# Kernel tuning notes

Hardware: AMD Instinct MI355X
Metric: run time of the kernel (lower is better)

## Reference

```python
import jax, jax.numpy as jnp
import numpy as np

D = 256      # d_model
SUB = 3      # number of adjacency subsets
GROUPS = 8
N, T, V = 32, 256, 19


def setup_inputs() -> dict:
    key = jax.random.key(0)
    ks = jax.random.split(key, 4)
    return {
        "x": jax.random.normal(ks[0], (N, T, V, D), jnp.float32),
        "para": jax.random.normal(ks[1], (3, GROUPS, V, V), jnp.float32),
        "linear_weight": jax.random.normal(ks[2], (D, D * SUB), jnp.float32) * 0.05,
        "linear_bias": jax.random.normal(ks[3], (1, D * SUB, 1, 1), jnp.float32) * 0.05,
        "bn_gamma": jnp.ones((D * SUB,), jnp.float32),
        "bn_beta": jnp.zeros((D * SUB,), jnp.float32),
        "bn1_gamma": jnp.ones((D,), jnp.float32),
        "bn1_beta": jnp.zeros((D,), jnp.float32),
    }


def _bn(x, gamma, beta, eps=1e-5):
    # BatchNorm2d (training mode): stats over (n, t, v) per channel
    m = jnp.mean(x, axis=(0, 2, 3), keepdims=True)
    v = jnp.var(x, axis=(0, 2, 3), keepdims=True)
    return (x - m) * jax.lax.rsqrt(v + eps) * gamma[None, :, None, None] + beta[None, :, None, None]


def reference(x, para, linear_weight, linear_bias, bn_gamma, bn_beta, bn1_gamma, bn1_beta):
    xc = jnp.transpose(x, (0, 3, 1, 2))                 # (n, c, t, v)
    # expand per-group adjacency to per-channel: (3, D, V, V)
    A = jnp.tile(para, (1, D // GROUPS, 1, 1))
    # L2 row-normalize along last dim (matches torch.norm(dim=-1))
    A = A / (jnp.linalg.norm(A, axis=-1, keepdims=True) + 1e-4)
    # channel mixing: (n, 3c, t, v)
    y = jnp.einsum('nctw,cd->ndtw', xc, linear_weight)
    y = _bn(y + linear_bias, bn_gamma, bn_beta)
    n, kc, t, v = y.shape
    y = y.reshape(n, SUB, kc // SUB, t, v)              # (n, k, c, t, v)
    # per-channel tiny 19x19 adjacency matmul
    y = jnp.einsum('nkctv,kcvw->nctw', y, A)            # (n, c, t, v)
    out = jax.nn.relu(_bn(y + xc, bn1_gamma, bn1_beta))
    return jnp.transpose(out, (0, 2, 3, 1))             # (n, t, v, c)
```

## Files before the change

kernel.cpp:

```cpp
#include <hip/hip_runtime.h>

typedef unsigned short u16;
typedef unsigned int u32;
typedef float f32x4 __attribute__((ext_vector_type(4)));
typedef __bf16 bf16x8 __attribute__((ext_vector_type(8)));

#define M_ALL 155648.0f
#define XP 264
#define YBP 152
#define ATP 72
#define ZBP 153

__device__ __forceinline__ u16 f2bf(float f) {
  union { float f; u32 u; } x; x.f = f;
  u32 u = x.u;
  u += 0x7FFFu + ((u >> 16) & 1u);
  return (u16)(u >> 16);
}
__device__ __forceinline__ float bf2f(u16 h) {
  union { u32 u; float f; } x; x.u = ((u32)h) << 16;
  return x.f;
}
__device__ __forceinline__ f32x4 zero4() { f32x4 z = {0.f, 0.f, 0.f, 0.f}; return z; }

__global__ void k_prep(const float* __restrict__ para, u16* __restrict__ wa,
                       float* __restrict__ stats) {
  int tid = threadIdx.x;
  for (int i = tid; i < 2048; i += 512) stats[i] = 0.f;
  if (tid < 456) {
    int k = tid / 152, rem = tid % 152, g = rem / 19, v = rem % 19;
    int base = ((k * 8 + g) * 19 + v) * 19;
    float ss = 0.f;
    #pragma unroll
    for (int w = 0; w < 19; ++w) { float a = para[base + w]; ss += a * a; }
    float inv = 1.f / (sqrtf(ss) + 1e-4f);
    #pragma unroll
    for (int w = 0; w < 19; ++w) wa[base + w] = f2bf(para[base + w] * inv);
  }
}

__global__ void k_wt(const float* __restrict__ W, u16* __restrict__ wt) {
  int idx = blockIdx.x * 512 + threadIdx.x;
  int d = idx >> 8, c = idx & 255;
  wt[idx] = f2bf(W[c * 768 + d]);
}

__global__ __launch_bounds__(512, 2) void k_stats(const float* __restrict__ x,
                                                  const u16* __restrict__ wt,
                                                  float* __restrict__ sumy) {
  __shared__ u16 xs[152 * XP];
  __shared__ float scr[768];
  int tid = threadIdx.x;
  int bid = blockIdx.x;
  int n = bid >> 5, tg = bid & 31;
  const float* xbase = x + (size_t)(n * 256 + tg * 8) * 4864;

  {
    int r = tid >> 6, c4 = (tid & 63) << 2;
    for (int it = 0; it < 19; ++it) {
      int m = it * 8 + r;
      float4 f = *reinterpret_cast<const float4*>(xbase + m * 256 + c4);
      uint2 p;
      p.x = (u32)f2bf(f.x) | ((u32)f2bf(f.y) << 16);
      p.y = (u32)f2bf(f.z) | ((u32)f2bf(f.w) << 16);
      *reinterpret_cast<uint2*>(&xs[m * XP + c4]) = p;
    }
  }
  __syncthreads();

  int lane = tid & 63, wave = tid >> 6;
  int mhalf = wave & 1, nt3 = wave >> 1;
  int cl = lane & 15, q = lane >> 4;
  const bf16x8* wtv = reinterpret_cast<const bf16x8*>(wt);
  int arow[5];
  #pragma unroll
  for (int i = 0; i < 5; ++i) {
    int rr = mhalf * 80 + i * 16 + cl;
    arow[i] = (rr > 151 ? 151 : rr) * XP;
  }
  float msk4 = (mhalf == 1 && q >= 2) ? 0.f : 1.f;

  for (int nc = 0; nc < 4; ++nc) {
    f32x4 acc[5][3];
    #pragma unroll
    for (int i = 0; i < 5; ++i)
      #pragma unroll
      for (int jj = 0; jj < 3; ++jj) acc[i][jj] = zero4();

    for (int s = 0; s < 8; ++s) {
      int kof = s * 32 + q * 8;
      bf16x8 b[3];
      #pragma unroll
      for (int jj = 0; jj < 3; ++jj) {
        int j = nt3 * 3 + jj;
        int d = (j >> 2) * 256 + nc * 64 + (j & 3) * 16 + cl;
        b[jj] = wtv[d * 32 + s * 4 + q];
      }
      #pragma unroll
      for (int i = 0; i < 5; ++i) {
        bf16x8 a = *reinterpret_cast<const bf16x8*>(&xs[arow[i] + kof]);
        #pragma unroll
        for (int jj = 0; jj < 3; ++jj)
          acc[i][jj] = __builtin_amdgcn_mfma_f32_16x16x32_bf16(a, b[jj], acc[i][jj], 0, 0, 0);
      }
    }
    #pragma unroll
    for (int jj = 0; jj < 3; ++jj) {
      float ps = 0.f, qs = 0.f;
      #pragma unroll
      for (int i = 0; i < 5; ++i) {
        float im = (i == 4) ? msk4 : 1.f;
        #pragma unroll
        for (int r = 0; r < 4; ++r) { float v = acc[i][jj][r] * im; ps += v; qs += v * v; }
      }
      ps += __shfl_xor(ps, 16); ps += __shfl_xor(ps, 32);
      qs += __shfl_xor(qs, 16); qs += __shfl_xor(qs, 32);
      if (lane < 16) { scr[wave * 96 + jj * 32 + lane] = ps; scr[wave * 96 + jj * 32 + 16 + lane] = qs; }
    }
    __syncthreads();
    if (tid < 384) {
      int nt = tid / 96, r = tid % 96, jj = r / 32, comp = (r & 31) >> 4, l = r & 15;
      int a0 = (2 * nt) * 96 + jj * 32 + comp * 16 + l;
      float val = scr[a0] + scr[a0 + 96];
      int j = nt * 3 + jj;
      int d = (j >> 2) * 256 + nc * 64 + (j & 3) * 16 + l;
      atomicAdd(&sumy[comp * 768 + d], val);
    }
    __syncthreads();
  }
}

__global__ void k_f1(const float* __restrict__ stats, const float* __restrict__ gam,
                     const float* __restrict__ bet, float* __restrict__ ST) {
  int d = threadIdx.x;
  float inv = 1.f / M_ALL;
  float mr = stats[d] * inv;
  float qv = stats[768 + d] * inv;
  float var = qv - mr * mr;
  float Sc = gam[d] * rsqrtf(var + 1e-5f);
  ST[d] = Sc;
  ST[768 + d] = bet[d] - mr * Sc;
}

__global__ __launch_bounds__(512, 2) void k_main(const float* __restrict__ x,
                                                 const u16* __restrict__ wt,
                                                 const u16* __restrict__ wa,
                                                 const float* __restrict__ ST,
                                                 float* __restrict__ sumz,
                                                 float* __restrict__ out) {
  __shared__ u16 xs[152 * XP];
  __shared__ u16 yb[3 * 64 * YBP];
  __shared__ u16 at[8 * 20 * ATP];
  int tid = threadIdx.x;
  int bid = blockIdx.x;
  int n = bid >> 5, tg = bid & 31;
  const float* xbase = x + (size_t)(n * 256 + tg * 8) * 4864;
  size_t obase = (size_t)(n * 256 + tg * 8) * 4864;

  for (int i = tid; i < 8 * 20 * ATP; i += 512) {
    int g = i / (20 * ATP), r = i % (20 * ATP), w = r / ATP, kv = r % ATP;
    u16 val = 0;
    if (w < 19 && kv < 57) {
      int k = kv / 19, v = kv - 19 * k;
      val = wa[((k * 8 + g) * 19 + v) * 19 + w];
    }
    at[i] = val;
  }
  {
    int r = tid >> 6, c4 = (tid & 63) << 2;
    for (int it = 0; it < 19; ++it) {
      int m = it * 8 + r;
      float4 f = *reinterpret_cast<const float4*>(xbase + m * 256 + c4);
      uint2 p;
      p.x = (u32)f2bf(f.x) | ((u32)f2bf(f.y) << 16);
      p.y = (u32)f2bf(f.z) | ((u32)f2bf(f.w) << 16);
      *reinterpret_cast<uint2*>(&xs[m * XP + c4]) = p;
    }
  }
  __syncthreads();

  int lane = tid & 63, wave = tid >> 6;
  int mhalf = wave & 1, nt3 = wave >> 1;
  int cl = lane & 15, q = lane >> 4;
  int g = wave;
  const bf16x8* wtv = reinterpret_cast<const bf16x8*>(wt);
  float* scrz = reinterpret_cast<float*>(&yb[9792]);
  u16* zbuf = yb;
  int arow[5];
  #pragma unroll
  for (int i = 0; i < 5; ++i) {
    int rr = mhalf * 80 + i * 16 + cl;
    arow[i] = (rr > 151 ? 151 : rr) * XP;
  }
  int aoff[2][8];
  #pragma unroll
  for (int ks = 0; ks < 2; ++ks)
    #pragma unroll
    for (int e = 0; e < 8; ++e) {
      int kv = ks * 32 + q * 8 + e;
      if (kv > 56) kv = 0;
      int k = kv / 19, v = kv - 19 * k;
      aoff[ks][e] = k * (64 * YBP) + v;
    }

  for (int nc = 0; nc < 4; ++nc) {
    f32x4 acc[5][3];
    #pragma unroll
    for (int i = 0; i < 5; ++i)
      #pragma unroll
      for (int jj = 0; jj < 3; ++jj) acc[i][jj] = zero4();
    for (int s = 0; s < 8; ++s) {
      int kof = s * 32 + q * 8;
      bf16x8 b[3];
      #pragma unroll
      for (int jj = 0; jj < 3; ++jj) {
        int j = nt3 * 3 + jj;
        int d = (j >> 2) * 256 + nc * 64 + (j & 3) * 16 + cl;
        b[jj] = wtv[d * 32 + s * 4 + q];
      }
      #pragma unroll
      for (int i = 0; i < 5; ++i) {
        bf16x8 a = *reinterpret_cast<const bf16x8*>(&xs[arow[i] + kof]);
        #pragma unroll
        for (int jj = 0; jj < 3; ++jj)
          acc[i][jj] = __builtin_amdgcn_mfma_f32_16x16x32_bf16(a, b[jj], acc[i][jj], 0, 0, 0);
      }
    }
    __syncthreads();

    #pragma unroll
    for (int jj = 0; jj < 3; ++jj) {
      int j = nt3 * 3 + jj;
      int ksub = j >> 2;
      int d = ksub * 256 + nc * 64 + (j & 3) * 16 + cl;
      float Sc = ST[d], Tc = ST[768 + d];
      int clloc = (j & 3) * 16 + cl;
      #pragma unroll
      for (int i = 0; i < 5; ++i) {
        int m = mhalf * 80 + i * 16 + q * 4;
        if (m < 152) {
          uint2 p;
          float v0 = acc[i][jj][0] * Sc + Tc;
          float v1 = acc[i][jj][1] * Sc + Tc;
          float v2 = acc[i][jj][2] * Sc + Tc;
          float v3 = acc[i][jj][3] * Sc + Tc;
          p.x = (u32)f2bf(v0) | ((u32)f2bf(v1) << 16);
          p.y = (u32)f2bf(v2) | ((u32)f2bf(v3) << 16);
          *reinterpret_cast<uint2*>(&yb[(ksub * 64 + clloc) * YBP + m]) = p;
        }
      }
    }
    __syncthreads();

    f32x4 zacc[4][2];
    #pragma unroll
    for (int mt = 0; mt < 4; ++mt) { zacc[mt][0] = zero4(); zacc[mt][1] = zero4(); }
    #pragma unroll
    for (int ks = 0; ks < 2; ++ks) {
      bf16x8 bfr[2];
      #pragma unroll
      for (int nt = 0; nt < 2; ++nt) {
        int w = nt * 16 + cl; if (w > 19) w = 19;
        bfr[nt] = *reinterpret_cast<const bf16x8*>(&at[(g * 20 + w) * ATP + ks * 32 + q * 8]);
      }
      #pragma unroll
      for (int mt = 0; mt < 4; ++mt) {
        int tc = mt * 16 + cl;
        int t = tc >> 3, c8 = tc & 7;
        int ybase = (c8 * 8 + g) * YBP + t * 19;
        union { bf16x8 v; u16 u[8]; } afr;
        #pragma unroll
        for (int e = 0; e < 8; ++e) afr.u[e] = yb[aoff[ks][e] + ybase];
        #pragma unroll
        for (int nt = 0; nt < 2; ++nt)
          zacc[mt][nt] = __builtin_amdgcn_mfma_f32_16x16x32_bf16(afr.v, bfr[nt], zacc[mt][nt], 0, 0, 0);
      }
    }
    __syncthreads();

    #pragma unroll
    for (int mt = 0; mt < 4; ++mt)
      #pragma unroll
      for (int nt = 0; nt < 2; ++nt)
        #pragma unroll
        for (int r = 0; r < 4; ++r) {
          int w = nt * 16 + cl;
          if (w < 19) {
            int tc = mt * 16 + q * 4 + r;
            int t = tc >> 3, c8 = tc & 7;
            zbuf[(c8 * 8 + g) * ZBP + t * 19 + w] = f2bf(zacc[mt][nt][r]);
          }
        }
    __syncthreads();

    float sz = 0.f, sq = 0.f;
    int cloc = tid & 63;
    int cglob = nc * 64 + cloc;
    #pragma unroll 1
    for (int rep = 0; rep < 19; ++rep) {
      int idx = rep * 512 + tid;
      int mp = idx >> 6;
      float z = bf2f(zbuf[cloc * ZBP + mp]) + bf2f(xs[mp * XP + cglob]);
      out[obase + (size_t)mp * 256 + cglob] = z;
      sz += z; sq += z * z;
    }
    scrz[cloc * 8 + (tid >> 6)] = sz;
    scrz[512 + cloc * 8 + (tid >> 6)] = sq;
    __syncthreads();
    if (tid < 128) {
      int comp = tid >> 6, c = tid & 63;
      float v = 0.f;
      #pragma unroll
      for (int h = 0; h < 8; ++h) v += scrz[comp * 512 + c * 8 + h];
      atomicAdd(&sumz[comp * 256 + nc * 64 + c], v);
    }
  }
}

__global__ void k_f2(const float* __restrict__ statz, const float* __restrict__ gam,
                     const float* __restrict__ bet, float* __restrict__ S1T1) {
  int c = threadIdx.x;
  float inv = 1.f / M_ALL;
  float mz = statz[c] * inv;
  float qv = statz[256 + c] * inv;
  float var = qv - mz * mz;
  float Sc = gam[c] * rsqrtf(var + 1e-5f);
  S1T1[c] = Sc;
  S1T1[256 + c] = bet[c] - mz * Sc;
}

__global__ __launch_bounds__(256) void k_relu(float* __restrict__ out,
                                              const float* __restrict__ S1T1) {
  int tid = threadIdx.x;
  int lane = tid & 63;
  int wv = ((blockIdx.x << 8) + tid) >> 6;
  const float4* s14 = reinterpret_cast<const float4*>(S1T1);
  float4 sv = s14[lane], tv = s14[64 + lane];
  float4* o4 = reinterpret_cast<float4*>(out);
  #pragma unroll 1
  for (int r = 0; r < 19; ++r) {
    size_t i = ((size_t)r * 8192 + wv) * 64 + lane;
    float4 f = o4[i];
    f.x = fmaxf(f.x * sv.x + tv.x, 0.f);
    f.y = fmaxf(f.y * sv.y + tv.y, 0.f);
    f.z = fmaxf(f.z * sv.z + tv.z, 0.f);
    f.w = fmaxf(f.w * sv.w + tv.w, 0.f);
    o4[i] = f;
  }
}

extern "C" void kernel_launch(void* const* d_in, const int* in_sizes, int n_in,
                              void* d_out, int out_size, void* d_ws, size_t ws_size,
                              hipStream_t stream) {
  const float* x    = (const float*)d_in[0];
  const float* para = (const float*)d_in[1];
  const float* W    = (const float*)d_in[2];
  const float* bng  = (const float*)d_in[4];
  const float* bnb  = (const float*)d_in[5];
  const float* bn1g = (const float*)d_in[6];
  const float* bn1b = (const float*)d_in[7];
  float* out = (float*)d_out;

  char* ws = (char*)d_ws;
  u16* wt    = (u16*)ws;
  u16* wa    = (u16*)(ws + 393216);
  float* st  = (float*)(ws + 410560);
  float* sumy = st;
  float* sumz = st + 1536;
  float* ST   = (float*)(ws + 418752);
  float* S1T1 = (float*)(ws + 424896);

  k_prep<<<dim3(1),    dim3(512), 0, stream>>>(para, wa, st);
  k_wt  <<<dim3(384),  dim3(512), 0, stream>>>(W, wt);
  k_stats<<<dim3(1024), dim3(512), 0, stream>>>(x, wt, sumy);
  k_f1  <<<dim3(1),    dim3(768), 0, stream>>>(sumy, bng, bnb, ST);
  k_main<<<dim3(1024), dim3(512), 0, stream>>>(x, wt, wa, ST, sumz, out);
  k_f2  <<<dim3(1),    dim3(256), 0, stream>>>(sumz, bn1g, bn1b, S1T1);
  k_relu<<<dim3(2048), dim3(256), 0, stream>>>(out, S1T1);
}
```

Baseline: 697.9 us.

## Compute first BN stats via Gram matrix of x and swizzle shared layouts

Replaces the statistics pass, which ran the full x·W GEMM just to get per-channel mean and variance, with a 256x256 Gram matrix of x plus column sums. Mean and variance of y are then derived as W^T colsum and w^T G w in small follow-up kernels (k_sym, k_f1). The main kernel also moves to XOR-swizzled LDS layouts for xs and for a new y2 buffer, so the adjacency-matmul A operand becomes one vector load instead of eight scalar gathers. The adjacency B fragments are preloaded into registers once. The risk is a different rounding path for the variance (bf16 Gram accumulated in fp32 with atomics) and the extra small kernels and memset.

```diff
diff --git a/kernel.cpp b/kernel.cpp
--- a/kernel.cpp
+++ b/kernel.cpp
@@ -6,10 +6,7 @@
 typedef __bf16 bf16x8 __attribute__((ext_vector_type(8)));
 
 #define M_ALL 155648.0f
-#define XP 264
-#define YBP 152
-#define ATP 72
-#define ZBP 153
+#define GP 168
 
 __device__ __forceinline__ u16 f2bf(float f) {
   union { float f; u32 u; } x; x.f = f;
@@ -23,10 +20,17 @@
 }
 __device__ __forceinline__ f32x4 zero4() { f32x4 z = {0.f, 0.f, 0.f, 0.f}; return z; }
 
-__global__ void k_prep(const float* __restrict__ para, u16* __restrict__ wa,
-                       float* __restrict__ stats) {
+__device__ __forceinline__ int xs_idx(int m, int c) {
+  return m * 256 + ((((c >> 3) ^ (m & 7)) << 3) | (c & 7));
+}
+__device__ __forceinline__ int y2_idx(int r, int kvp) {
+  int sw = (r & 7) ^ ((r >> 3) & 7);
+  return r * 64 + ((((kvp >> 3) ^ sw) << 3) | (kvp & 7));
+}
+
+__global__ void k_prep(const float* __restrict__ para, u16* __restrict__ wa2) {
+  __shared__ float aL[3 * 8 * 19 * 19];
   int tid = threadIdx.x;
-  for (int i = tid; i < 2048; i += 512) stats[i] = 0.f;
   if (tid < 456) {
     int k = tid / 152, rem = tid % 152, g = rem / 19, v = rem % 19;
     int base = ((k * 8 + g) * 19 + v) * 19;
@@ -35,7 +39,17 @@
     for (int w = 0; w < 19; ++w) { float a = para[base + w]; ss += a * a; }
     float inv = 1.f / (sqrtf(ss) + 1e-4f);
     #pragma unroll
-    for (int w = 0; w < 19; ++w) wa[base + w] = f2bf(para[base + w] * inv);
+    for (int w = 0; w < 19; ++w) aL[base + w] = para[base + w] * inv;
+  }
+  __syncthreads();
+  for (int i = tid; i < 8 * 20 * 64; i += 512) {
+    int g = i / 1280, rem = i % 1280, w = rem >> 6, kvp = rem & 63;
+    u16 val = 0;
+    if (w < 19 && kvp < 57) {
+      int k = kvp / 19, v = kvp - 19 * k;
+      val = f2bf(aL[((k * 8 + g) * 19 + v) * 19 + w]);
+    }
+    wa2[i] = val;
   }
 }
 
@@ -45,15 +59,129 @@
   wt[idx] = f2bf(W[c * 768 + d]);
 }
 
-__global__ __launch_bounds__(512, 2) void k_stats(const float* __restrict__ x,
-                                                  const u16* __restrict__ wt,
-                                                  float* __restrict__ sumy) {
-  __shared__ u16 xs[152 * XP];
-  __shared__ float scr[768];
+__global__ __launch_bounds__(512, 2) void k_gram(const float* __restrict__ x,
+                                                 float* __restrict__ G,
+                                                 float* __restrict__ colsum) {
+  __shared__ u16 xsT[256 * GP];
+  __shared__ float scs[512];
+  int tid = threadIdx.x, bid = blockIdx.x;
+  int c = tid & 255, mh = tid >> 8;
+  int lane = tid & 63, wave = tid >> 6;
+  int cl = lane & 15, q = lane >> 4;
+
+  if (tid < 256) {
+    *reinterpret_cast<uint2*>(&xsT[tid * GP + 152]) = make_uint2(0u, 0u);
+    *reinterpret_cast<uint2*>(&xsT[tid * GP + 156]) = make_uint2(0u, 0u);
+  }
+
+  float cs = 0.f;
+  f32x4 acc[2][16];
+  #pragma unroll
+  for (int ri = 0; ri < 2; ++ri)
+    #pragma unroll
+    for (int j = 0; j < 16; ++j) acc[ri][j] = zero4();
+
+  for (int ss = 0; ss < 4; ++ss) {
+    int sl = bid * 4 + ss;
+    const float* xb = x + (size_t)sl * 152 * 256;
+    __syncthreads();
+    #pragma unroll 1
+    for (int it = 0; it < 19; ++it) {
+      int m0 = it * 8 + mh * 4;
+      float v0 = xb[(m0 + 0) * 256 + c];
+      float v1 = xb[(m0 + 1) * 256 + c];
+      float v2 = xb[(m0 + 2) * 256 + c];
+      float v3 = xb[(m0 + 3) * 256 + c];
+      cs += v0 + v1 + v2 + v3;
+      uint2 p;
+      p.x = (u32)f2bf(v0) | ((u32)f2bf(v1) << 16);
+      p.y = (u32)f2bf(v2) | ((u32)f2bf(v3) << 16);
+      *reinterpret_cast<uint2*>(&xsT[c * GP + m0]) = p;
+    }
+    __syncthreads();
+    #pragma unroll
+    for (int s = 0; s < 5; ++s) {
+      int kof = s * 32 + q * 8;
+      bf16x8 a0 = *reinterpret_cast<const bf16x8*>(&xsT[(wave * 16 + cl) * GP + kof]);
+      bf16x8 a1 = *reinterpret_cast<const bf16x8*>(&xsT[((wave + 8) * 16 + cl) * GP + kof]);
+      #pragma unroll
+      for (int ct2 = 0; ct2 < 16; ++ct2) {
+        bf16x8 b = *reinterpret_cast<const bf16x8*>(&xsT[(ct2 * 16 + cl) * GP + kof]);
+        acc[0][ct2] = __builtin_amdgcn_mfma_f32_16x16x32_bf16(a0, b, acc[0][ct2], 0, 0, 0);
+        acc[1][ct2] = __builtin_amdgcn_mfma_f32_16x16x32_bf16(a1, b, acc[1][ct2], 0, 0, 0);
+      }
+    }
+  }
+  #pragma unroll
+  for (int ri = 0; ri < 2; ++ri) {
+    int ct = wave + ri * 8;
+    #pragma unroll
+    for (int ct2 = 0; ct2 < 16; ++ct2) {
+      if (ct2 >= ct) {
+        #pragma unroll
+        for (int r4 = 0; r4 < 4; ++r4)
+          atomicAdd(&G[(ct * 16 + q * 4 + r4) * 256 + ct2 * 16 + cl], acc[ri][ct2][r4]);
+      }
+    }
+  }
+  scs[tid] = cs;
+  __syncthreads();
+  if (tid < 256) atomicAdd(&colsum[tid], scs[tid] + scs[tid + 256]);
+}
+
+__global__ void k_sym(float* __restrict__ G) {
+  int i = blockIdx.x * 256 + threadIdx.x;
+  int r = i >> 8, cN = i & 255;
+  if (r > cN) G[i] = G[cN * 256 + r];
+}
+
+__global__ __launch_bounds__(256) void k_f1(const float* __restrict__ G,
+                                            const float* __restrict__ colsum,
+                                            const float* __restrict__ W,
+                                            const float* __restrict__ gam,
+                                            const float* __restrict__ bet,
+                                            float* __restrict__ ST) {
+  __shared__ float wd[256];
+  __shared__ float red[16];
+  int d = blockIdx.x, c = threadIdx.x;
+  float wv = W[c * 768 + d];
+  wd[c] = wv;
+  __syncthreads();
+  float dot = 0.f;
+  const float* Gr = G + c * 256;
+  #pragma unroll 4
+  for (int j = 0; j < 256; ++j) dot += Gr[j] * wd[j];
+  float part = wv * dot;
+  float mpart = colsum[c] * wv;
+  #pragma unroll
+  for (int o = 32; o; o >>= 1) { part += __shfl_down(part, o); mpart += __shfl_down(mpart, o); }
+  int lane = c & 63, w = c >> 6;
+  if (lane == 0) { red[w] = part; red[8 + w] = mpart; }
+  __syncthreads();
+  if (c == 0) {
+    float qv = red[0] + red[1] + red[2] + red[3];
+    float ms = red[8] + red[9] + red[10] + red[11];
+    float mean = ms / M_ALL;
+    float var = qv / M_ALL - mean * mean;
+    float S = gam[d] * rsqrtf(var + 1e-5f);
+    ST[d] = S;
+    ST[768 + d] = bet[d] - mean * S;
+  }
+}
+
+__global__ __launch_bounds__(512, 2) void k_main(const float* __restrict__ x,
+                                                 const u16* __restrict__ wt,
+                                                 const u16* __restrict__ wa2,
+                                                 const float* __restrict__ ST,
+                                                 float* __restrict__ sumz,
+                                                 float* __restrict__ out) {
+  __shared__ u16 xs[152 * 256];
+  __shared__ u16 y2[512 * 64];
+  __shared__ float scrz[1024];
   int tid = threadIdx.x;
   int bid = blockIdx.x;
-  int n = bid >> 5, tg = bid & 31;
-  const float* xbase = x + (size_t)(n * 256 + tg * 8) * 4864;
+  const float* xbase = x + (size_t)bid * 152 * 256;
+  size_t obase = (size_t)bid * 152 * 256;
 
   {
     int r = tid >> 6, c4 = (tid & 63) << 2;
@@ -63,145 +191,34 @@
       uint2 p;
       p.x = (u32)f2bf(f.x) | ((u32)f2bf(f.y) << 16);
       p.y = (u32)f2bf(f.z) | ((u32)f2bf(f.w) << 16);
-      *reinterpret_cast<uint2*>(&xs[m * XP + c4]) = p;
-    }
-  }
-  __syncthreads();
-
-  int lane = tid & 63, wave = tid >> 6;
-  int mhalf = wave & 1, nt3 = wave >> 1;
-  int cl = lane & 15, q = lane >> 4;
-  const bf16x8* wtv = reinterpret_cast<const bf16x8*>(wt);
-  int arow[5];
-  #pragma unroll
-  for (int i = 0; i < 5; ++i) {
-    int rr = mhalf * 80 + i * 16 + cl;
-    arow[i] = (rr > 151 ? 151 : rr) * XP;
-  }
-  float msk4 = (mhalf == 1 && q >= 2) ? 0.f : 1.f;
-
-  for (int nc = 0; nc < 4; ++nc) {
-    f32x4 acc[5][3];
-    #pragma unroll
-    for (int i = 0; i < 5; ++i)
-      #pragma unroll
-      for (int jj = 0; jj < 3; ++jj) acc[i][jj] = zero4();
-
-    for (int s = 0; s < 8; ++s) {
-      int kof = s * 32 + q * 8;
-      bf16x8 b[3];
-      #pragma unroll
-      for (int jj = 0; jj < 3; ++jj) {
-        int j = nt3 * 3 + jj;
-        int d = (j >> 2) * 256 + nc * 64 + (j & 3) * 16 + cl;
-        b[jj] = wtv[d * 32 + s * 4 + q];
-      }
-      #pragma unroll
-      for (int i = 0; i < 5; ++i) {
-        bf16x8 a = *reinterpret_cast<const bf16x8*>(&xs[arow[i] + kof]);
-        #pragma unroll
-        for (int jj = 0; jj < 3; ++jj)
-          acc[i][jj] = __builtin_amdgcn_mfma_f32_16x16x32_bf16(a, b[jj], acc[i][jj], 0, 0, 0);
-      }
-    }
-    #pragma unroll
-    for (int jj = 0; jj < 3; ++jj) {
-      float ps = 0.f, qs = 0.f;
-      #pragma unroll
-      for (int i = 0; i < 5; ++i) {
-        float im = (i == 4) ? msk4 : 1.f;
-        #pragma unroll
-        for (int r = 0; r < 4; ++r) { float v = acc[i][jj][r] * im; ps += v; qs += v * v; }
-      }
-      ps += __shfl_xor(ps, 16); ps += __shfl_xor(ps, 32);
-      qs += __shfl_xor(qs, 16); qs += __shfl_xor(qs, 32);
-      if (lane < 16) { scr[wave * 96 + jj * 32 + lane] = ps; scr[wave * 96 + jj * 32 + 16 + lane] = qs; }
-    }
-    __syncthreads();
-    if (tid < 384) {
-      int nt = tid / 96, r = tid % 96, jj = r / 32, comp = (r & 31) >> 4, l = r & 15;
-      int a0 = (2 * nt) * 96 + jj * 32 + comp * 16 + l;
-      float val = scr[a0] + scr[a0 + 96];
-      int j = nt * 3 + jj;
-      int d = (j >> 2) * 256 + nc * 64 + (j & 3) * 16 + l;
-      atomicAdd(&sumy[comp * 768 + d], val);
-    }
-    __syncthreads();
-  }
-}
-
-__global__ void k_f1(const float* __restrict__ stats, const float* __restrict__ gam,
-                     const float* __restrict__ bet, float* __restrict__ ST) {
-  int d = threadIdx.x;
-  float inv = 1.f / M_ALL;
-  float mr = stats[d] * inv;
-  float qv = stats[768 + d] * inv;
-  float var = qv - mr * mr;
-  float Sc = gam[d] * rsqrtf(var + 1e-5f);
-  ST[d] = Sc;
-  ST[768 + d] = bet[d] - mr * Sc;
-}
-
-__global__ __launch_bounds__(512, 2) void k_main(const float* __restrict__ x,
-                                                 const u16* __restrict__ wt,
-                                                 const u16* __restrict__ wa,
-                                                 const float* __restrict__ ST,
-                                                 float* __restrict__ sumz,
-                                                 float* __restrict__ out) {
-  __shared__ u16 xs[152 * XP];
-  __shared__ u16 yb[3 * 64 * YBP];
-  __shared__ u16 at[8 * 20 * ATP];
-  int tid = threadIdx.x;
-  int bid = blockIdx.x;
-  int n = bid >> 5, tg = bid & 31;
-  const float* xbase = x + (size_t)(n * 256 + tg * 8) * 4864;
-  size_t obase = (size_t)(n * 256 + tg * 8) * 4864;
-
-  for (int i = tid; i < 8 * 20 * ATP; i += 512) {
-    int g = i / (20 * ATP), r = i % (20 * ATP), w = r / ATP, kv = r % ATP;
-    u16 val = 0;
-    if (w < 19 && kv < 57) {
-      int k = kv / 19, v = kv - 19 * k;
-      val = wa[((k * 8 + g) * 19 + v) * 19 + w];
-    }
-    at[i] = val;
-  }
-  {
-    int r = tid >> 6, c4 = (tid & 63) << 2;
-    for (int it = 0; it < 19; ++it) {
-      int m = it * 8 + r;
-      float4 f = *reinterpret_cast<const float4*>(xbase + m * 256 + c4);
-      uint2 p;
-      p.x = (u32)f2bf(f.x) | ((u32)f2bf(f.y) << 16);
-      p.y = (u32)f2bf(f.z) | ((u32)f2bf(f.w) << 16);
-      *reinterpret_cast<uint2*>(&xs[m * XP + c4]) = p;
-    }
-  }
-  __syncthreads();
+      *reinterpret_cast<uint2*>(&xs[xs_idx(m, c4)]) = p;
+    }
+  }
 
   int lane = tid & 63, wave = tid >> 6;
   int mhalf = wave & 1, nt3 = wave >> 1;
   int cl = lane & 15, q = lane >> 4;
   int g = wave;
   const bf16x8* wtv = reinterpret_cast<const bf16x8*>(wt);
-  float* scrz = reinterpret_cast<float*>(&yb[9792]);
-  u16* zbuf = yb;
-  int arow[5];
+  float* zbufF = reinterpret_cast<float*>(y2);
+
+  bf16x8 bfr[2][2];
+  #pragma unroll
+  for (int ks = 0; ks < 2; ++ks)
+    #pragma unroll
+    for (int nt = 0; nt < 2; ++nt) {
+      int w = nt * 16 + cl; int wc = (w < 20) ? w : 19;
+      bfr[ks][nt] = *reinterpret_cast<const bf16x8*>(&wa2[(g * 20 + wc) * 64 + ks * 32 + q * 8]);
+    }
+
+  int arow[5], mlow[5];
   #pragma unroll
   for (int i = 0; i < 5; ++i) {
     int rr = mhalf * 80 + i * 16 + cl;
-    arow[i] = (rr > 151 ? 151 : rr) * XP;
-  }
-  int aoff[2][8];
-  #pragma unroll
-  for (int ks = 0; ks < 2; ++ks)
-    #pragma unroll
-    for (int e = 0; e < 8; ++e) {
-      int kv = ks * 32 + q * 8 + e;
-      if (kv > 56) kv = 0;
-      int k = kv / 19, v = kv - 19 * k;
-      aoff[ks][e] = k * (64 * YBP) + v;
-    }
+    if (rr > 151) rr = 151;
+    arow[i] = rr * 256; mlow[i] = rr & 7;
+  }
+  __syncthreads();
 
   for (int nc = 0; nc < 4; ++nc) {
     f32x4 acc[5][3];
@@ -210,17 +227,17 @@
       #pragma unroll
       for (int jj = 0; jj < 3; ++jj) acc[i][jj] = zero4();
     for (int s = 0; s < 8; ++s) {
-      int kof = s * 32 + q * 8;
+      int sq4 = s * 4 + q;
       bf16x8 b[3];
       #pragma unroll
       for (int jj = 0; jj < 3; ++jj) {
         int j = nt3 * 3 + jj;
         int d = (j >> 2) * 256 + nc * 64 + (j & 3) * 16 + cl;
-        b[jj] = wtv[d * 32 + s * 4 + q];
+        b[jj] = wtv[d * 32 + sq4];
       }
       #pragma unroll
       for (int i = 0; i < 5; ++i) {
-        bf16x8 a = *reinterpret_cast<const bf16x8*>(&xs[arow[i] + kof]);
+        bf16x8 a = *reinterpret_cast<const bf16x8*>(&xs[arow[i] + ((sq4 ^ mlow[i]) << 3)]);
         #pragma unroll
         for (int jj = 0; jj < 3; ++jj)
           acc[i][jj] = __builtin_amdgcn_mfma_f32_16x16x32_bf16(a, b[jj], acc[i][jj], 0, 0, 0);
@@ -229,24 +246,29 @@
     __syncthreads();
 
     #pragma unroll
+    for (int kk = 0; kk < 7; ++kk)
+      y2[y2_idx(tid, 57 + kk)] = 0;
+
+    #pragma unroll
     for (int jj = 0; jj < 3; ++jj) {
       int j = nt3 * 3 + jj;
       int ksub = j >> 2;
-      int d = ksub * 256 + nc * 64 + (j & 3) * 16 + cl;
+      int c_local = (j & 3) * 16 + cl;
+      int d = ksub * 256 + nc * 64 + c_local;
       float Sc = ST[d], Tc = ST[768 + d];
-      int clloc = (j & 3) * 16 + cl;
       #pragma unroll
       for (int i = 0; i < 5; ++i) {
-        int m = mhalf * 80 + i * 16 + q * 4;
-        if (m < 152) {
-          uint2 p;
-          float v0 = acc[i][jj][0] * Sc + Tc;
-          float v1 = acc[i][jj][1] * Sc + Tc;
-          float v2 = acc[i][jj][2] * Sc + Tc;
-          float v3 = acc[i][jj][3] * Sc + Tc;
-          p.x = (u32)f2bf(v0) | ((u32)f2bf(v1) << 16);
-          p.y = (u32)f2bf(v2) | ((u32)f2bf(v3) << 16);
-          *reinterpret_cast<uint2*>(&yb[(ksub * 64 + clloc) * YBP + m]) = p;
+        int mb = mhalf * 80 + i * 16 + q * 4;
+        #pragma unroll
+        for (int r4 = 0; r4 < 4; ++r4) {
+          int m = mb + r4;
+          if (m < 152) {
+            int t = (m * 27) >> 9;
+            int v = m - t * 19;
+            int kvp = ksub * 19 + v;
+            int r = t * 64 + c_local;
+            y2[y2_idx(r, kvp)] = f2bf(acc[i][jj][r4] * Sc + Tc);
+          }
         }
       }
     }
@@ -257,23 +279,16 @@
     for (int mt = 0; mt < 4; ++mt) { zacc[mt][0] = zero4(); zacc[mt][1] = zero4(); }
     #pragma unroll
     for (int ks = 0; ks < 2; ++ks) {
-      bf16x8 bfr[2];
-      #pragma unroll
-      for (int nt = 0; nt < 2; ++nt) {
-        int w = nt * 16 + cl; if (w > 19) w = 19;
-        bfr[nt] = *reinterpret_cast<const bf16x8*>(&at[(g * 20 + w) * ATP + ks * 32 + q * 8]);
-      }
       #pragma unroll
       for (int mt = 0; mt < 4; ++mt) {
         int tc = mt * 16 + cl;
         int t = tc >> 3, c8 = tc & 7;
-        int ybase = (c8 * 8 + g) * YBP + t * 19;
-        union { bf16x8 v; u16 u[8]; } afr;
-        #pragma unroll
-        for (int e = 0; e < 8; ++e) afr.u[e] = yb[aoff[ks][e] + ybase];
+        int r = t * 64 + c8 * 8 + g;
+        int ch = (ks * 4 + q) ^ g ^ c8;
+        bf16x8 afr = *reinterpret_cast<const bf16x8*>(&y2[r * 64 + (ch << 3)]);
         #pragma unroll
         for (int nt = 0; nt < 2; ++nt)
-          zacc[mt][nt] = __builtin_amdgcn_mfma_f32_16x16x32_bf16(afr.v, bfr[nt], zacc[mt][nt], 0, 0, 0);
+          zacc[mt][nt] = __builtin_amdgcn_mfma_f32_16x16x32_bf16(afr, bfr[ks][nt], zacc[mt][nt], 0, 0, 0);
       }
     }
     __syncthreads();
@@ -281,16 +296,17 @@
     #pragma unroll
     for (int mt = 0; mt < 4; ++mt)
       #pragma unroll
-      for (int nt = 0; nt < 2; ++nt)
-        #pragma unroll
-        for (int r = 0; r < 4; ++r) {
-          int w = nt * 16 + cl;
-          if (w < 19) {
-            int tc = mt * 16 + q * 4 + r;
-            int t = tc >> 3, c8 = tc & 7;
-            zbuf[(c8 * 8 + g) * ZBP + t * 19 + w] = f2bf(zacc[mt][nt][r]);
+      for (int nt = 0; nt < 2; ++nt) {
+        int w = nt * 16 + cl;
+        if (w < 19) {
+          #pragma unroll
+          for (int r4 = 0; r4 < 4; ++r4) {
+            int mm = mt * 16 + q * 4 + r4;
+            int t = mm >> 3, c8 = mm & 7;
+            zbufF[(c8 * 8 + g) * 153 + t * 19 + w] = zacc[mt][nt][r4];
           }
         }
+      }
     __syncthreads();
 
     float sz = 0.f, sq = 0.f;
@@ -298,20 +314,19 @@
     int cglob = nc * 64 + cloc;
     #pragma unroll 1
     for (int rep = 0; rep < 19; ++rep) {
-      int idx = rep * 512 + tid;
-      int mp = idx >> 6;
-      float z = bf2f(zbuf[cloc * ZBP + mp]) + bf2f(xs[mp * XP + cglob]);
+      int mp = rep * 8 + (tid >> 6);
+      float z = zbufF[cloc * 153 + mp] + bf2f(xs[xs_idx(mp, cglob)]);
       out[obase + (size_t)mp * 256 + cglob] = z;
       sz += z; sq += z * z;
     }
-    scrz[cloc * 8 + (tid >> 6)] = sz;
-    scrz[512 + cloc * 8 + (tid >> 6)] = sq;
+    scrz[(tid >> 6) * 64 + cloc] = sz;
+    scrz[512 + (tid >> 6) * 64 + cloc] = sq;
     __syncthreads();
     if (tid < 128) {
       int comp = tid >> 6, c = tid & 63;
       float v = 0.f;
       #pragma unroll
-      for (int h = 0; h < 8; ++h) v += scrz[comp * 512 + c * 8 + h];
+      for (int h = 0; h < 8; ++h) v += scrz[comp * 512 + h * 64 + c];
       atomicAdd(&sumz[comp * 256 + nc * 64 + c], v);
     }
   }
@@ -362,19 +377,21 @@
   float* out = (float*)d_out;
 
   char* ws = (char*)d_ws;
-  u16* wt    = (u16*)ws;
-  u16* wa    = (u16*)(ws + 393216);
-  float* st  = (float*)(ws + 410560);
-  float* sumy = st;
-  float* sumz = st + 1536;
-  float* ST   = (float*)(ws + 418752);
-  float* S1T1 = (float*)(ws + 424896);
-
-  k_prep<<<dim3(1),    dim3(512), 0, stream>>>(para, wa, st);
+  u16* wt     = (u16*)ws;
+  u16* wa2    = (u16*)(ws + 393216);
+  float* G    = (float*)(ws + 413696);
+  float* csum = (float*)(ws + 675840);
+  float* sumz = (float*)(ws + 676864);
+  float* ST   = (float*)(ws + 678912);
+  float* S1T1 = (float*)(ws + 685056);
+
+  hipMemsetAsync(ws + 413696, 0, 262144 + 1024 + 2048, stream);
+  k_prep<<<dim3(1),    dim3(512), 0, stream>>>(para, wa2);
   k_wt  <<<dim3(384),  dim3(512), 0, stream>>>(W, wt);
-  k_stats<<<dim3(1024), dim3(512), 0, stream>>>(x, wt, sumy);
-  k_f1  <<<dim3(1),    dim3(768), 0, stream>>>(sumy, bng, bnb, ST);
-  k_main<<<dim3(1024), dim3(512), 0, stream>>>(x, wt, wa, ST, sumz, out);
+  k_gram<<<dim3(256),  dim3(512), 0, stream>>>(x, G, csum);
+  k_sym <<<dim3(256),  dim3(256), 0, stream>>>(G);
+  k_f1  <<<dim3(768),  dim3(256), 0, stream>>>(G, csum, W, bng, bnb, ST);
+  k_main<<<dim3(1024), dim3(512), 0, stream>>>(x, wt, wa2, ST, sumz, out);
   k_f2  <<<dim3(1),    dim3(256), 0, stream>>>(sumz, bn1g, bn1b, S1T1);
   k_relu<<<dim3(2048), dim3(256), 0, stream>>>(out, S1T1);
 }
```

Result: faster. 628.8 us (-9.9%).
